# Kernel optimization log

Hardware: AMD Instinct MI355X
Metric: run time of the kernel (lower is better)

## Reference

```python
import jax, jax.numpy as jnp
import numpy as np

H = 2048        # hidden_size
NH = 16         # num query heads
NKV = 4         # num kv heads
HD = 128        # head_dim
EPS = 1e-6
SCALE = HD ** -0.5
GROUPS = NH // NKV


def rotate_half(x):
    x1, x2 = x[..., : HD // 2], x[..., HD // 2:]
    return jnp.concatenate((-x2, x1), axis=-1)


def rmsnorm(x, w):
    # x: [..., HD]
    var = jnp.mean(jnp.square(x), axis=-1, keepdims=True)
    return x * jax.lax.rsqrt(var + EPS) * w


def setup_inputs() -> dict:
    key = jax.random.key(0)
    ks = jax.random.split(key, 10)
    B, QL, CL = 4, 1024, 3072
    s = 0.02
    return {
        "noise": jax.random.normal(ks[0], (B, QL, H), jnp.float32),
        "ctx": jax.random.normal(ks[1], (B, CL, H), jnp.float32),
        "cos": jax.random.uniform(ks[2], (B, CL + QL, HD), jnp.float32, -1.0, 1.0),
        "sin": jax.random.uniform(ks[3], (B, CL + QL, HD), jnp.float32, -1.0, 1.0),
        "Wq": jax.random.normal(ks[4], (H, NH * HD), jnp.float32) * s,
        "Wk": jax.random.normal(ks[5], (H, NKV * HD), jnp.float32) * s,
        "Wv": jax.random.normal(ks[6], (H, NKV * HD), jnp.float32) * s,
        "Wo": jax.random.normal(ks[7], (NH * HD, H), jnp.float32) * s,
        "qn_w": jnp.ones((HD,), jnp.float32),
        "kn_w": jnp.ones((HD,), jnp.float32),
    }


def reference(noise, ctx, cos, sin, Wq, Wk, Wv, Wo, qn_w, kn_w):
    B, QL, _ = noise.shape
    CL = ctx.shape[1]
    KL = CL + QL

    # Q from noise
    q = (noise @ Wq).reshape(B, QL, NH, HD)
    q = rmsnorm(q, qn_w).transpose(0, 2, 1, 3)            # [B, NH, QL, HD]

    # K/V from [ctx ; noise]
    kv_in = jnp.concatenate([ctx, noise], axis=1)          # [B, KL, H]
    k = (kv_in @ Wk).reshape(B, KL, NKV, HD)
    k = rmsnorm(k, kn_w).transpose(0, 2, 1, 3)             # [B, NKV, KL, HD]
    v = (kv_in @ Wv).reshape(B, KL, NKV, HD).transpose(0, 2, 1, 3)

    # RoPE: queries use last QL positions
    cos_q, sin_q = cos[:, -QL:, None].transpose(0, 2, 1, 3), sin[:, -QL:, None].transpose(0, 2, 1, 3)
    cos_k, sin_k = cos[:, None], sin[:, None]
    q = q * cos_q + rotate_half(q) * sin_q
    k = k * cos_k + rotate_half(k) * sin_k

    # GQA expansion
    k = jnp.repeat(k, GROUPS, axis=1)                      # [B, NH, KL, HD]
    v = jnp.repeat(v, GROUPS, axis=1)

    attn = jnp.einsum('bhqd,bhkd->bhqk', q, k) * SCALE     # [B, NH, QL, KL]
    attn = jax.nn.softmax(attn.astype(jnp.float32), axis=-1).astype(v.dtype)
    out = jnp.einsum('bhqk,bhkd->bhqd', attn, v)
    out = out.transpose(0, 2, 1, 3).reshape(B, QL, NH * HD)
    return out @ Wo
```

## Files before the change

kernel.cpp:

```cpp
#include <hip/hip_runtime.h>
#include <cstdint>
#include <cstddef>

#define DEVI __device__ __forceinline__

typedef short bf16x8 __attribute__((ext_vector_type(8)));
typedef short bf16x4 __attribute__((ext_vector_type(4)));
typedef float f32x4  __attribute__((ext_vector_type(4)));

constexpr int H_  = 2048;
constexpr int NH  = 16;
constexpr int NKV = 4;
constexpr int HD  = 128;
constexpr int B_  = 4;
constexpr int QL  = 1024;
constexpr int CL  = 3072;
constexpr int KL  = 4096;
constexpr float EPS = 1e-6f;
constexpr float SCALE_LOG2E = 0.08838834764831845f * 1.4426950408889634f;

DEVI unsigned short f2bf(float x) {
  unsigned int u = __float_as_uint(x);
  u += 0x7FFFu + ((u >> 16) & 1u);
  return (unsigned short)(u >> 16);
}
DEVI float bf2f(unsigned short u) {
  return __uint_as_float(((unsigned int)u) << 16);
}
DEVI unsigned cvtpk(float a, float b) {
  unsigned r;
  asm("v_cvt_pk_bf16_f32 %0, %1, %2" : "=v"(r) : "v"(a), "v"(b));
  return r;
}
DEVI bf16x4 mk4(float a, float b, float c, float d) {
  union { unsigned u[2]; bf16x4 v; } r;
  r.u[0] = cvtpk(a, b);
  r.u[1] = cvtpk(c, d);
  return r.v;
}

DEVI void async16(const void* g, void* l) {
  __builtin_amdgcn_global_load_lds(
      (const __attribute__((address_space(1))) void*)g,
      (__attribute__((address_space(3))) void*)l, 16, 0, 0);
}

__global__ __launch_bounds__(256)
void prep(const float* __restrict__ noise, const float* __restrict__ ctx,
          unsigned short* __restrict__ kvin) {
  const size_t t = (size_t)blockIdx.x * 256 + threadIdx.x;
  const size_t e = t * 8;
  const int row = (int)(e / H_), col = (int)(e % H_);
  const int b = row >> 12, pos = row & 4095;
  const float* src = (pos < CL) ? ctx + ((size_t)(b * CL + pos)) * H_ + col
                                : noise + ((size_t)(b * QL + (pos - CL))) * H_ + col;
  float4 x = ((const float4*)src)[0], y = ((const float4*)src)[1];
  bf16x8 v;
  v[0] = (short)f2bf(x.x); v[1] = (short)f2bf(x.y);
  v[2] = (short)f2bf(x.z); v[3] = (short)f2bf(x.w);
  v[4] = (short)f2bf(y.x); v[5] = (short)f2bf(y.y);
  v[6] = (short)f2bf(y.z); v[7] = (short)f2bf(y.w);
  *(bf16x8*)(kvin + e) = v;
}

__global__ __launch_bounds__(256)
void wtrans(const float* __restrict__ in, unsigned short* __restrict__ out,
            int K, int N) {
  __shared__ float t[64][65];
  const int ktiles = K >> 6;
  const int kt = blockIdx.x % ktiles;
  const int nt = blockIdx.x / ktiles;
  {
    const int r = threadIdx.x >> 2, cs = threadIdx.x & 3;
    const float4* src = (const float4*)(in + (size_t)(kt * 64 + r) * N + nt * 64 + cs * 16);
    #pragma unroll
    for (int i = 0; i < 4; ++i) {
      float4 v = src[i];
      t[r][cs * 16 + i * 4 + 0] = v.x;
      t[r][cs * 16 + i * 4 + 1] = v.y;
      t[r][cs * 16 + i * 4 + 2] = v.z;
      t[r][cs * 16 + i * 4 + 3] = v.w;
    }
  }
  __syncthreads();
  {
    const int n = threadIdx.x >> 2, ks = threadIdx.x & 3;
    bf16x8 o0, o1;
    #pragma unroll
    for (int i = 0; i < 8; ++i) o0[i] = (short)f2bf(t[ks * 16 + i][n]);
    #pragma unroll
    for (int i = 0; i < 8; ++i) o1[i] = (short)f2bf(t[ks * 16 + 8 + i][n]);
    unsigned short* op = out + (size_t)(nt * 64 + n) * K + kt * 64 + ks * 16;
    *(bf16x8*)(op) = o0;
    *(bf16x8*)(op + 8) = o1;
  }
}

template <int MODE>
__global__ __launch_bounds__(256)
void gemm2(const unsigned short* __restrict__ Abf,
           const unsigned short* __restrict__ Bt,
           const float* __restrict__ normw,
           const float* __restrict__ cosb, const float* __restrict__ sinb,
           unsigned short* __restrict__ outb, float* __restrict__ outf) {
  constexpr int M  = (MODE == 1 || MODE == 2) ? (B_ * KL) : (B_ * QL);
  constexpr int K  = H_;
  constexpr int MT = M / 128;

  __shared__ union U {
    struct { unsigned short a[128][64]; unsigned short b[128][64]; } st;
    unsigned short ct[128][138];
  } sm;

  const int tid  = threadIdx.x;
  const int tm   = blockIdx.x % MT;
  const int tn   = blockIdx.x / MT;
  const int wid  = tid >> 6, lane = tid & 63, quad = lane >> 4, lm = lane & 15;
  const int wm   = wid >> 1, wn = wid & 1;

  f32x4 acc[4][4];
  #pragma unroll
  for (int i = 0; i < 4; ++i)
    #pragma unroll
    for (int j = 0; j < 4; ++j)
      #pragma unroll
      for (int r = 0; r < 4; ++r) acc[i][j][r] = 0.f;

  const unsigned short* agp[4];
  const unsigned short* bgp[4];
  #pragma unroll
  for (int i = 0; i < 4; ++i) {
    const int idx = i * 256 + tid;
    const int arow = idx >> 3, g = idx & 7, gg = g ^ (arow & 7);
    int grow;
    if constexpr (MODE == 0) {
      const int gmr = tm * 128 + arow;
      grow = (gmr >> 10) * KL + CL + (gmr & 1023);
    } else {
      grow = tm * 128 + arow;
    }
    agp[i] = Abf + (size_t)grow * K + gg * 8;
    bgp[i] = Bt + (size_t)(tn * 128 + arow) * K + gg * 8;
  }

  for (int kt = 0; kt < K / 64; ++kt) {
    __syncthreads();
    #pragma unroll
    for (int i = 0; i < 4; ++i) {
      async16(agp[i] + kt * 64, (char*)&sm.st.a[0][0] + (i * 256 + wid * 64) * 16);
      async16(bgp[i] + kt * 64, (char*)&sm.st.b[0][0] + (i * 256 + wid * 64) * 16);
    }
    __syncthreads();
    #pragma unroll
    for (int ks = 0; ks < 2; ++ks) {
      bf16x8 af[4], bfr[4];
      #pragma unroll
      for (int i = 0; i < 4; ++i) {
        const int swz = (ks * 4 + quad) ^ (lm & 7);
        af[i] = *(const bf16x8*)&sm.st.a[wm * 64 + i * 16 + lm][swz * 8];
      }
      #pragma unroll
      for (int j = 0; j < 4; ++j) {
        const int swz = (ks * 4 + quad) ^ (lm & 7);
        bfr[j] = *(const bf16x8*)&sm.st.b[wn * 64 + j * 16 + lm][swz * 8];
      }
      #pragma unroll
      for (int i = 0; i < 4; ++i)
        #pragma unroll
        for (int j = 0; j < 4; ++j)
          acc[i][j] = __builtin_amdgcn_mfma_f32_16x16x32_bf16(af[i], bfr[j], acc[i][j], 0, 0, 0);
    }
  }

  if constexpr (MODE == 3) {
    #pragma unroll
    for (int i = 0; i < 4; ++i)
      #pragma unroll
      for (int j = 0; j < 4; ++j) {
        const int row = tm * 128 + wm * 64 + i * 16 + quad * 4;
        const int col = tn * 128 + wn * 64 + j * 16 + lm;
        #pragma unroll
        for (int rr = 0; rr < 4; ++rr)
          outf[(size_t)(row + rr) * H_ + col] = acc[i][j][rr];
      }
    return;
  }

  __syncthreads();
  #pragma unroll
  for (int i = 0; i < 4; ++i)
    #pragma unroll
    for (int j = 0; j < 4; ++j)
      #pragma unroll
      for (int rr = 0; rr < 4; ++rr)
        sm.ct[wm * 64 + i * 16 + quad * 4 + rr][wn * 64 + j * 16 + lm] =
            f2bf(acc[i][j][rr]);
  __syncthreads();

  const int row2 = tid >> 1, half = tid & 1;
  if constexpr (MODE == 0 || MODE == 1) {
    const int gmr = tm * 128 + row2;
    int ci; size_t obase;
    if constexpr (MODE == 0) {
      const int b = gmr >> 10, pos = gmr & 1023;
      ci = (b * KL + CL + pos) * HD;
      obase = ((size_t)((b * NH + tn) * QL + pos)) * HD;
    } else {
      const int b = gmr >> 12, pos = gmr & 4095;
      ci = (b * KL + pos) * HD;
      obase = ((size_t)((b * NKV + tn) * KL + pos)) * HD;
    }
    float ss = 0.f;
    for (int d = half * 64; d < half * 64 + 64; ++d) {
      float v = bf2f(sm.ct[row2][d]);
      ss += v * v;
    }
    ss += __shfl_xor(ss, 1);
    const float rinv = rsqrtf(ss * (1.0f / 128.0f) + EPS);
    constexpr float OSC = (MODE == 0) ? SCALE_LOG2E : 1.0f;
    #pragma unroll
    for (int d8 = 0; d8 < 8; ++d8) {
      bf16x8 v;
      #pragma unroll
      for (int j = 0; j < 8; ++j) {
        const int d = half * 64 + d8 * 8 + j;
        const float x  = bf2f(sm.ct[row2][d])      * rinv * normw[d];
        const float xo = bf2f(sm.ct[row2][d ^ 64]) * rinv * normw[d ^ 64];
        const float rot = (d < 64) ? -xo : xo;
        v[j] = (short)f2bf((x * cosb[ci + d] + rot * sinb[ci + d]) * OSC);
      }
      *(bf16x8*)(outb + obase + half * 64 + d8 * 8) = v;
    }
  } else {
    const int d = row2;
    const int b = (tm * 128) >> 12;
    const int posBase = ((tm * 128) & 4095) + half * 64;
    const size_t obase = ((size_t)((b * NKV + tn) * HD + d)) * KL + posBase;
    #pragma unroll
    for (int k8 = 0; k8 < 8; ++k8) {
      bf16x8 v;
      #pragma unroll
      for (int j = 0; j < 8; ++j)
        v[j] = (short)sm.ct[half * 64 + k8 * 8 + j][d];
      *(bf16x8*)(outb + obase + k8 * 8) = v;
    }
  }
}

__global__ __launch_bounds__(256, 1)
void attn2(const unsigned short* __restrict__ qb,
           const unsigned short* __restrict__ kb,
           const unsigned short* __restrict__ vtb,
           unsigned short* __restrict__ ao) {
  __shared__ unsigned short kl[2][64][128];
  __shared__ unsigned short vl[2][128][64];

  const int tid = threadIdx.x;
  const int wave = tid >> 6, lane = tid & 63, quad = lane >> 4, lm = lane & 15;
  const int qblk = blockIdx.x & 3;
  const int bh = blockIdx.x >> 2;
  const int b = bh >> 4, h = bh & 15, kvh = h >> 2;
  const int q0 = qblk * 256 + wave * 64;

  bf16x8 qf[4][4];
  const unsigned short* qbase = qb + ((size_t)((b * NH + h) * QL + q0)) * HD;
  #pragma unroll
  for (int t = 0; t < 4; ++t)
    #pragma unroll
    for (int kq = 0; kq < 4; ++kq)
      qf[t][kq] = *(const bf16x8*)(qbase + (t * 16 + lm) * HD + kq * 32 + quad * 8);

  f32x4 o[4][8];
  float li[4] = {0.f, 0.f, 0.f, 0.f};
  #pragma unroll
  for (int t = 0; t < 4; ++t)
    #pragma unroll
    for (int dt = 0; dt < 8; ++dt)
      #pragma unroll
      for (int rr = 0; rr < 4; ++rr) o[t][dt][rr] = 0.f;

  const unsigned short* kbase = kb + ((size_t)(b * NKV + kvh)) * KL * HD;
  const unsigned short* vbase = vtb + ((size_t)(b * NKV + kvh)) * HD * KL;

  const int krow0 = tid >> 4, kgc = tid & 15;
  const int kgg = (kgc & 8) | ((kgc & 7) ^ (krow0 & 7));
  const unsigned short* kgp0 = kbase + (size_t)krow0 * HD + kgg * 8;
  const int vrow0 = tid >> 3;
  const int vgv = (tid & 7) ^ (vrow0 & 7);
  const unsigned short* vgp0 = vbase + (size_t)vrow0 * KL + vgv * 8;

  auto stage = [&](int bufi, int ktt) {
    #pragma unroll
    for (int i = 0; i < 4; ++i) {
      async16(kgp0 + (size_t)ktt * (64 * HD) + i * (16 * HD),
              (char*)&kl[bufi][0][0] + (i * 256 + wave * 64) * 16);
      async16(vgp0 + (size_t)ktt * 64 + i * (32 * KL),
              (char*)&vl[bufi][0][0] + (i * 256 + wave * 64) * 16);
    }
  };

  stage(0, 0);
  for (int kt = 0; kt < KL / 64; ++kt) {
    const int cur = kt & 1;
    if (kt + 1 < KL / 64) {
      stage(cur ^ 1, kt + 1);
      asm volatile("s_waitcnt vmcnt(8)" ::: "memory");
    } else {
      asm volatile("s_waitcnt vmcnt(0)" ::: "memory");
    }
    __builtin_amdgcn_s_barrier();

    #pragma unroll
    for (int j = 0; j < 2; ++j) {
      bf16x8 kf[2][4];
      #pragma unroll
      for (int sub = 0; sub < 2; ++sub) {
        const int nt = j * 2 + sub;
        #pragma unroll
        for (int kq = 0; kq < 4; ++kq) {
          const int gc = kq * 4 + quad;
          const int swz = (gc & 8) | ((gc & 7) ^ (lm & 7));
          kf[sub][kq] = *(const bf16x8*)&kl[cur][nt * 16 + lm][swz * 8];
        }
      }
      f32x4 s[4][2];
      #pragma unroll
      for (int t = 0; t < 4; ++t)
        #pragma unroll
        for (int sub = 0; sub < 2; ++sub)
          #pragma unroll
          for (int rr = 0; rr < 4; ++rr) s[t][sub][rr] = 0.f;
      __builtin_amdgcn_s_setprio(1);
      #pragma unroll
      for (int kq = 0; kq < 4; ++kq)
        #pragma unroll
        for (int sub = 0; sub < 2; ++sub)
          #pragma unroll
          for (int t = 0; t < 4; ++t)
            s[t][sub] = __builtin_amdgcn_mfma_f32_16x16x32_bf16(
                kf[sub][kq], qf[t][kq], s[t][sub], 0, 0, 0);
      __builtin_amdgcn_s_setprio(0);

      bf16x8 vfr[8];
      #pragma unroll
      for (int dt = 0; dt < 8; ++dt) {
        const int gv = (j * 4 + quad) ^ (lm & 7);
        vfr[dt] = *(const bf16x8*)&vl[cur][dt * 16 + lm][gv * 8];
      }

      bf16x8 P[4];
      #pragma unroll
      for (int t = 0; t < 4; ++t) {
        float e00 = __builtin_amdgcn_exp2f(s[t][0][0]);
        float e01 = __builtin_amdgcn_exp2f(s[t][0][1]);
        float e02 = __builtin_amdgcn_exp2f(s[t][0][2]);
        float e03 = __builtin_amdgcn_exp2f(s[t][0][3]);
        float e10 = __builtin_amdgcn_exp2f(s[t][1][0]);
        float e11 = __builtin_amdgcn_exp2f(s[t][1][1]);
        float e12 = __builtin_amdgcn_exp2f(s[t][1][2]);
        float e13 = __builtin_amdgcn_exp2f(s[t][1][3]);
        li[t] += ((e00 + e01) + (e02 + e03)) + ((e10 + e11) + (e12 + e13));
        unsigned A0 = cvtpk(e00, e01), A1 = cvtpk(e02, e03);
        unsigned B0 = cvtpk(e10, e11), B1 = cvtpk(e12, e13);
        asm volatile("v_permlane32_swap_b32 %0, %1" : "+v"(A0), "+v"(B0));
        asm volatile("v_permlane32_swap_b32 %0, %1" : "+v"(A1), "+v"(B1));
        asm volatile("v_permlane16_swap_b32 %0, %1" : "+v"(A0), "+v"(B0));
        asm volatile("v_permlane16_swap_b32 %0, %1" : "+v"(A1), "+v"(B1));
        union { unsigned u[4]; bf16x8 v; } up;
        up.u[0] = A0; up.u[1] = A1; up.u[2] = B0; up.u[3] = B1;
        P[t] = up.v;
      }

      __builtin_amdgcn_s_setprio(1);
      #pragma unroll
      for (int dt = 0; dt < 8; ++dt)
        #pragma unroll
        for (int t = 0; t < 4; ++t)
          o[t][dt] = __builtin_amdgcn_mfma_f32_16x16x32_bf16(
              vfr[dt], P[t], o[t][dt], 0, 0, 0);
      __builtin_amdgcn_s_setprio(0);
    }
    __builtin_amdgcn_s_barrier();
  }

  #pragma unroll
  for (int t = 0; t < 4; ++t) {
    float l = li[t];
    l += __shfl_xor(l, 16);
    l += __shfl_xor(l, 32);
    const float inv = 1.0f / l;
    const size_t rowbase = ((size_t)(b * QL + q0 + t * 16 + lm)) * (NH * HD) + h * HD;
    #pragma unroll
    for (int dt = 0; dt < 8; ++dt) {
      bf16x4 v = mk4(o[t][dt][0] * inv, o[t][dt][1] * inv,
                     o[t][dt][2] * inv, o[t][dt][3] * inv);
      *(bf16x4*)(ao + rowbase + dt * 16 + quad * 4) = v;
    }
  }
}

extern "C" void kernel_launch(void* const* d_in, const int* in_sizes, int n_in,
                              void* d_out, int out_size, void* d_ws, size_t ws_size,
                              hipStream_t stream) {
  const float* noise = (const float*)d_in[0];
  const float* ctx   = (const float*)d_in[1];
  const float* cosb  = (const float*)d_in[2];
  const float* sinb  = (const float*)d_in[3];
  const float* Wq    = (const float*)d_in[4];
  const float* Wk    = (const float*)d_in[5];
  const float* Wv    = (const float*)d_in[6];
  const float* Wo    = (const float*)d_in[7];
  const float* qn    = (const float*)d_in[8];
  const float* kn    = (const float*)d_in[9];
  float* out = (float*)d_out;

  char* ws = (char*)d_ws;
  unsigned short* kvin = (unsigned short*)(ws);
  unsigned short* aob  = (unsigned short*)(ws);
  unsigned short* WqT  = (unsigned short*)(ws + 67108864);
  unsigned short* WkT  = (unsigned short*)(ws + 67108864 + 8388608);
  unsigned short* WvT  = (unsigned short*)(ws + 67108864 + 10485760);
  unsigned short* WoT  = (unsigned short*)(ws + 67108864 + 12582912);
  unsigned short* qbuf = (unsigned short*)(ws + 67108864 + 20971520);
  unsigned short* kbuf = (unsigned short*)(ws + 67108864 + 37748736);
  unsigned short* vtb  = (unsigned short*)(ws + 67108864 + 54525952);

  prep<<<dim3((B_ * KL * H_) / 8 / 256), dim3(256), 0, stream>>>(noise, ctx, kvin);

  wtrans<<<dim3(1024), dim3(256), 0, stream>>>(Wq, WqT, 2048, 2048);
  wtrans<<<dim3(256),  dim3(256), 0, stream>>>(Wk, WkT, 2048, 512);
  wtrans<<<dim3(256),  dim3(256), 0, stream>>>(Wv, WvT, 2048, 512);
  wtrans<<<dim3(1024), dim3(256), 0, stream>>>(Wo, WoT, 2048, 2048);

  gemm2<0><<<dim3(32 * 16), dim3(256), 0, stream>>>(
      kvin, WqT, qn, cosb, sinb, qbuf, nullptr);
  gemm2<1><<<dim3(128 * 4), dim3(256), 0, stream>>>(
      kvin, WkT, kn, cosb, sinb, kbuf, nullptr);
  gemm2<2><<<dim3(128 * 4), dim3(256), 0, stream>>>(
      kvin, WvT, nullptr, nullptr, nullptr, vtb, nullptr);

  attn2<<<dim3(256), dim3(256), 0, stream>>>(qbuf, kbuf, vtb, aob);

  gemm2<3><<<dim3(32 * 16), dim3(256), 0, stream>>>(
      aob, WoT, nullptr, nullptr, nullptr, nullptr, out);
}
```

Measured before the change: 614.5 us.

## Halve attention query tile to double grid and vectorize norm-RoPE epilogue

```diff
diff --git a/kernel.cpp b/kernel.cpp
--- a/kernel.cpp
+++ b/kernel.cpp
@@ -107,9 +107,9 @@
   constexpr int K  = H_;
   constexpr int MT = M / 128;
 
-  __shared__ union U {
+  __shared__ union alignas(16) U {
     struct { unsigned short a[128][64]; unsigned short b[128][64]; } st;
-    unsigned short ct[128][138];
+    unsigned short ct[128][136];
   } sm;
 
   const int tid  = threadIdx.x;
@@ -210,26 +210,39 @@
       ci = (b * KL + pos) * HD;
       obase = ((size_t)((b * NKV + tn) * KL + pos)) * HD;
     }
+    const unsigned short* ctr = &sm.ct[row2][0];
     float ss = 0.f;
-    for (int d = half * 64; d < half * 64 + 64; ++d) {
-      float v = bf2f(sm.ct[row2][d]);
-      ss += v * v;
+    #pragma unroll
+    for (int i = 0; i < 8; ++i) {
+      bf16x8 v = *(const bf16x8*)(ctr + half * 64 + i * 8);
+      #pragma unroll
+      for (int jj = 0; jj < 8; ++jj) {
+        const float f = bf2f((unsigned short)v[jj]);
+        ss += f * f;
+      }
     }
     ss += __shfl_xor(ss, 1);
     const float rinv = rsqrtf(ss * (1.0f / 128.0f) + EPS);
     constexpr float OSC = (MODE == 0) ? SCALE_LOG2E : 1.0f;
     #pragma unroll
     for (int d8 = 0; d8 < 8; ++d8) {
-      bf16x8 v;
-      #pragma unroll
-      for (int j = 0; j < 8; ++j) {
-        const int d = half * 64 + d8 * 8 + j;
-        const float x  = bf2f(sm.ct[row2][d])      * rinv * normw[d];
-        const float xo = bf2f(sm.ct[row2][d ^ 64]) * rinv * normw[d ^ 64];
-        const float rot = (d < 64) ? -xo : xo;
-        v[j] = (short)f2bf((x * cosb[ci + d] + rot * sinb[ci + d]) * OSC);
-      }
-      *(bf16x8*)(outb + obase + half * 64 + d8 * 8) = v;
+      const int dbase = half * 64 + d8 * 8;
+      bf16x8 xv = *(const bf16x8*)(ctr + dbase);
+      bf16x8 xo = *(const bf16x8*)(ctr + (dbase ^ 64));
+      union { float4 v[2]; float f[8]; } cc, sn;
+      cc.v[0] = *(const float4*)(cosb + ci + dbase);
+      cc.v[1] = *(const float4*)(cosb + ci + dbase + 4);
+      sn.v[0] = *(const float4*)(sinb + ci + dbase);
+      sn.v[1] = *(const float4*)(sinb + ci + dbase + 4);
+      bf16x8 outv;
+      #pragma unroll
+      for (int jj = 0; jj < 8; ++jj) {
+        const float x  = bf2f((unsigned short)xv[jj]) * rinv * normw[dbase + jj];
+        const float xr = bf2f((unsigned short)xo[jj]) * rinv * normw[(dbase ^ 64) + jj];
+        const float rot = (half == 0) ? -xr : xr;
+        outv[jj] = (short)f2bf((x * cc.f[jj] + rot * sn.f[jj]) * OSC);
+      }
+      *(bf16x8*)(outb + obase + dbase) = outv;
     }
   } else {
     const int d = row2;
@@ -247,7 +260,7 @@
   }
 }
 
-__global__ __launch_bounds__(256, 1)
+__global__ __launch_bounds__(256, 2)
 void attn2(const unsigned short* __restrict__ qb,
            const unsigned short* __restrict__ kb,
            const unsigned short* __restrict__ vtb,
@@ -257,23 +270,23 @@
 
   const int tid = threadIdx.x;
   const int wave = tid >> 6, lane = tid & 63, quad = lane >> 4, lm = lane & 15;
-  const int qblk = blockIdx.x & 3;
-  const int bh = blockIdx.x >> 2;
+  const int qblk = blockIdx.x & 7;
+  const int bh = blockIdx.x >> 3;
   const int b = bh >> 4, h = bh & 15, kvh = h >> 2;
-  const int q0 = qblk * 256 + wave * 64;
-
-  bf16x8 qf[4][4];
+  const int q0 = qblk * 128 + wave * 32;
+
+  bf16x8 qf[2][4];
   const unsigned short* qbase = qb + ((size_t)((b * NH + h) * QL + q0)) * HD;
   #pragma unroll
-  for (int t = 0; t < 4; ++t)
+  for (int t = 0; t < 2; ++t)
     #pragma unroll
     for (int kq = 0; kq < 4; ++kq)
       qf[t][kq] = *(const bf16x8*)(qbase + (t * 16 + lm) * HD + kq * 32 + quad * 8);
 
-  f32x4 o[4][8];
-  float li[4] = {0.f, 0.f, 0.f, 0.f};
-  #pragma unroll
-  for (int t = 0; t < 4; ++t)
+  f32x4 o[2][8];
+  float li[2] = {0.f, 0.f};
+  #pragma unroll
+  for (int t = 0; t < 2; ++t)
     #pragma unroll
     for (int dt = 0; dt < 8; ++dt)
       #pragma unroll
@@ -323,9 +336,9 @@
           kf[sub][kq] = *(const bf16x8*)&kl[cur][nt * 16 + lm][swz * 8];
         }
       }
-      f32x4 s[4][2];
-      #pragma unroll
-      for (int t = 0; t < 4; ++t)
+      f32x4 s[2][2];
+      #pragma unroll
+      for (int t = 0; t < 2; ++t)
         #pragma unroll
         for (int sub = 0; sub < 2; ++sub)
           #pragma unroll
@@ -336,7 +349,7 @@
         #pragma unroll
         for (int sub = 0; sub < 2; ++sub)
           #pragma unroll
-          for (int t = 0; t < 4; ++t)
+          for (int t = 0; t < 2; ++t)
             s[t][sub] = __builtin_amdgcn_mfma_f32_16x16x32_bf16(
                 kf[sub][kq], qf[t][kq], s[t][sub], 0, 0, 0);
       __builtin_amdgcn_s_setprio(0);
@@ -348,9 +361,9 @@
         vfr[dt] = *(const bf16x8*)&vl[cur][dt * 16 + lm][gv * 8];
       }
 
-      bf16x8 P[4];
-      #pragma unroll
-      for (int t = 0; t < 4; ++t) {
+      bf16x8 P[2];
+      #pragma unroll
+      for (int t = 0; t < 2; ++t) {
         float e00 = __builtin_amdgcn_exp2f(s[t][0][0]);
         float e01 = __builtin_amdgcn_exp2f(s[t][0][1]);
         float e02 = __builtin_amdgcn_exp2f(s[t][0][2]);
@@ -375,7 +388,7 @@
       #pragma unroll
       for (int dt = 0; dt < 8; ++dt)
         #pragma unroll
-        for (int t = 0; t < 4; ++t)
+        for (int t = 0; t < 2; ++t)
           o[t][dt] = __builtin_amdgcn_mfma_f32_16x16x32_bf16(
               vfr[dt], P[t], o[t][dt], 0, 0, 0);
       __builtin_amdgcn_s_setprio(0);
@@ -384,7 +397,7 @@
   }
 
   #pragma unroll
-  for (int t = 0; t < 4; ++t) {
+  for (int t = 0; t < 2; ++t) {
     float l = li[t];
     l += __shfl_xor(l, 16);
     l += __shfl_xor(l, 32);
@@ -439,7 +452,7 @@
   gemm2<2><<<dim3(128 * 4), dim3(256), 0, stream>>>(
       kvin, WvT, nullptr, nullptr, nullptr, vtb, nullptr);
 
-  attn2<<<dim3(256), dim3(256), 0, stream>>>(qbuf, kbuf, vtb, aob);
+  attn2<<<dim3(512), dim3(256), 0, stream>>>(qbuf, kbuf, vtb, aob);
 
   gemm2<3><<<dim3(32 * 16), dim3(256), 0, stream>>>(
       aob, WoT, nullptr, nullptr, nullptr, nullptr, out);
```

After: 580.0 us. 5.6% less time.
